# Kernel optimization log

Measured on AMD Instinct MI355X. Metric: run time of the kernel, lower is better.

## Reference

```python
import jax, jax.numpy as jnp
import numpy as np


def conv(x, w, b=None, stride=1, pad=0):
    out = jax.lax.conv_general_dilated(x, w, (stride, stride), [(pad, pad), (pad, pad)],
                                       dimension_numbers=('NCHW', 'OIHW', 'NCHW'))
    if b is not None:
        out = out + b[None, :, None, None]
    return out


def fsm(x, att_w, conv_w):
    # FeatureSelectionModule: global-avg-pool -> 1x1 conv -> sigmoid gate, residual, 1x1 proj
    gap = jnp.mean(x, axis=(2, 3), keepdims=True)
    atten = jax.nn.sigmoid(conv(gap, att_w))
    return conv(x + x * atten, conv_w)


def mdcn(x, offset, mask, weight, bias, pad=1, G=8):
    # Modulated deformable conv v2: stride 1, dilation 1, conv groups 1, G deformable groups.
    N, C, H, W = x.shape
    Co, Ci, kh, kw = weight.shape
    K = kh * kw
    Cg = C // G
    off = offset.reshape(N, G, 2, K, H, W)          # per-group (y, x) offsets per kernel tap
    msk = mask.reshape(N, G, 1, K, H, W)
    ky, kx = jnp.meshgrid(jnp.arange(kh), jnp.arange(kw), indexing='ij')
    py = (jnp.arange(H, dtype=x.dtype)[None, None, None, :, None] - pad) + ky.reshape(1, 1, K, 1, 1) + off[:, :, 0]
    px = (jnp.arange(W, dtype=x.dtype)[None, None, None, None, :] - pad) + kx.reshape(1, 1, K, 1, 1) + off[:, :, 1]
    y0 = jnp.floor(py)
    x0 = jnp.floor(px)
    wy1 = py - y0
    wy0 = 1.0 - wy1
    wx1 = px - x0
    wx0 = 1.0 - wx1
    xg = x.reshape(N, G, Cg, H * W)

    def gather(iy, ix):
        valid = (iy >= 0) & (iy <= H - 1) & (ix >= 0) & (ix <= W - 1)
        idx = (jnp.clip(iy, 0, H - 1) * W + jnp.clip(ix, 0, W - 1)).astype(jnp.int32)
        v = jnp.take_along_axis(xg, idx.reshape(N, G, 1, K * H * W), axis=3)
        return v.reshape(N, G, Cg, K, H, W) * valid[:, :, None].astype(x.dtype)

    val = ((wy0 * wx0)[:, :, None] * gather(y0, x0)
         + (wy0 * wx1)[:, :, None] * gather(y0, x0 + 1)
         + (wy1 * wx0)[:, :, None] * gather(y0 + 1, x0)
         + (wy1 * wx1)[:, :, None] * gather(y0 + 1, x0 + 1))
    val = val * msk                                   # [N,G,Cg,K,H,W]
    out = jnp.einsum('ngckhw,ogck->nohw', val, weight.reshape(Co, G, Cg, K))
    return out + bias[None, :, None, None]


def align(feat_l, feat_s, att_w, fsm_w, off_w, om_w, om_b, dcn_w, dcn_b):
    # FeatureAlign_V2
    N, Cs, H, W = feat_s.shape[0], feat_s.shape[1], feat_l.shape[2], feat_l.shape[3]
    feat_up = jax.image.resize(feat_s, (N, Cs, H, W), 'bilinear')  # align_corners=False
    feat_arm = fsm(feat_l, att_w, fsm_w)
    off_feat = conv(jnp.concatenate([feat_arm, feat_up * 2.0], axis=1), off_w)
    om = conv(off_feat, om_w, om_b, pad=1)            # conv_offset_mask: 3*G*K channels
    o1, o2, mk = jnp.split(om, 3, axis=1)
    offset = jnp.concatenate([o1, o2], axis=1)
    mask = jax.nn.sigmoid(mk)
    feat_align = jax.nn.relu(mdcn(feat_up, offset, mask, dcn_w, dcn_b))
    return feat_align + feat_arm


def setup_inputs() -> dict:
    key = jax.random.key(0)
    ks = iter(jax.random.split(key, 64))

    def w(shape):
        fan_in = shape[1] * shape[2] * shape[3]
        return jax.random.normal(next(ks), shape, jnp.float32) / np.float32(np.sqrt(fan_in))

    def b(n):
        return jnp.zeros((n,), jnp.float32)

    d = {}
    d['c2'] = jax.random.normal(next(ks), (1, 256, 128, 128), jnp.float32)
    d['c3'] = jax.random.normal(next(ks), (1, 512, 64, 64), jnp.float32)
    d['c4'] = jax.random.normal(next(ks), (1, 1024, 32, 32), jnp.float32)
    d['c5'] = jax.random.normal(next(ks), (1, 2048, 16, 16), jnp.float32)
    OC = 256
    OM = 8 * 3 * 9  # deformable_groups * (2 offsets + 1 mask) * k*k = 216
    for tag, in_nc in (('16', 1024), ('8', 512), ('4', 256)):
        d['att_w' + tag] = w((in_nc, in_nc, 1, 1))
        d['fsm_w' + tag] = w((OC, in_nc, 1, 1))
        d['off_w' + tag] = w((OC, 2 * OC, 1, 1))
        d['om_w' + tag] = w((OM, OC, 3, 3))
        d['om_b' + tag] = b(OM)
        d['dcn_w' + tag] = w((OC, OC, 3, 3))
        d['dcn_b' + tag] = b(OC)
        d['out_w' + tag] = w((OC, OC, 3, 3))
        d['out_b' + tag] = b(OC)
    d['lat_w'] = w((OC, 2048, 1, 1))
    d['lat_b'] = b(OC)
    return d


def reference(c2, c3, c4, c5,
              att_w16, fsm_w16, off_w16, om_w16, om_b16, dcn_w16, dcn_b16, out_w16, out_b16,
              att_w8, fsm_w8, off_w8, om_w8, om_b8, dcn_w8, dcn_b8, out_w8, out_b8,
              att_w4, fsm_w4, off_w4, om_w4, om_b4, dcn_w4, dcn_b4, out_w4, out_b4,
              lat_w, lat_b):
    # top-down pass, coarsest first (matches FAN.forward with reversed inputs)
    p5 = conv(c5, lat_w, lat_b)
    f16 = align(c4, p5, att_w16, fsm_w16, off_w16, om_w16, om_b16, dcn_w16, dcn_b16)
    p4 = conv(f16, out_w16, out_b16, pad=1)
    f8 = align(c3, f16, att_w8, fsm_w8, off_w8, om_w8, om_b8, dcn_w8, dcn_b8)
    p3 = conv(f8, out_w8, out_b8, pad=1)
    f4 = align(c2, f8, att_w4, fsm_w4, off_w4, om_w4, om_b4, dcn_w4, dcn_b4)
    p2 = conv(f4, out_w4, out_b4, pad=1)
    return (p2, p3, p4, p5)
```

## Files before the change

kernel.cpp:

```cpp
#include <hip/hip_runtime.h>
#include <hip/hip_bf16.h>

typedef __hip_bfloat16 bf16;
typedef __attribute__((ext_vector_type(8))) short bf16x8;
typedef __attribute__((ext_vector_type(4))) float floatx4;

__device__ __forceinline__ float b2f(bf16 v) { return __bfloat162float(v); }
__device__ __forceinline__ bf16 f2b(float v) { return __float2bfloat16(v); }
__device__ __forceinline__ float us2f(unsigned short u) {
  union { unsigned int i; float f; } v; v.i = ((unsigned int)u) << 16; return v.f;
}
__device__ __forceinline__ unsigned short f2us(float f) {
  bf16 h = f2b(f); return *(unsigned short*)&h;
}

__global__ __launch_bounds__(256) void gap_kernel(const float* __restrict__ x,
                                                  float* __restrict__ gap,
                                                  int HW, float inv) {
  int c = blockIdx.x;
  const float* p = x + (size_t)c * HW;
  float s = 0.f;
  for (int i = threadIdx.x; i < HW; i += 256) s += p[i];
  __shared__ float red[256];
  red[threadIdx.x] = s;
  __syncthreads();
  for (int w = 128; w > 0; w >>= 1) {
    if (threadIdx.x < w) red[threadIdx.x] += red[threadIdx.x + w];
    __syncthreads();
  }
  if (threadIdx.x == 0) gap[c] = red[0] * inv;
}

__global__ __launch_bounds__(256) void atten_kernel(const float* __restrict__ w,
                                                    const float* __restrict__ gap,
                                                    float* __restrict__ scale, int Ci) {
  int wave = threadIdx.x >> 6, lane = threadIdx.x & 63;
  int o = blockIdx.x * 4 + wave;
  const float4* wr = (const float4*)(w + (size_t)o * Ci);
  const float4* g4 = (const float4*)gap;
  int n4 = Ci >> 2;
  float s = 0.f;
  for (int i = lane; i < n4; i += 64) {
    float4 a = wr[i], b = g4[i];
    s += a.x * b.x + a.y * b.y + a.z * b.z + a.w * b.w;
  }
#pragma unroll
  for (int off = 32; off > 0; off >>= 1) s += __shfl_down(s, off);
  if (lane == 0) scale[o] = 1.f + 1.f / (1.f + expf(-s));
}

__global__ __launch_bounds__(256) void upsample2x_nhwc_kernel(
    const bf16* __restrict__ src, bf16* __restrict__ dst, int Hs, int Ws) {
  int p = blockIdx.x;
  int c = threadIdx.x;
  int W = Ws * 2;
  int y = p / W, x = p - y * W;
  float fy = y * 0.5f - 0.25f;
  float fx = x * 0.5f - 0.25f;
  int y0 = (int)floorf(fy), x0 = (int)floorf(fx);
  float wy1 = fy - (float)y0, wx1 = fx - (float)x0;
  int y0c = min(max(y0, 0), Hs - 1);
  int y1c = min(max(y0 + 1, 0), Hs - 1);
  int x0c = min(max(x0, 0), Ws - 1);
  int x1c = min(max(x0 + 1, 0), Ws - 1);
  float v00 = b2f(src[(size_t)(y0c * Ws + x0c) * 256 + c]);
  float v01 = b2f(src[(size_t)(y0c * Ws + x1c) * 256 + c]);
  float v10 = b2f(src[(size_t)(y1c * Ws + x0c) * 256 + c]);
  float v11 = b2f(src[(size_t)(y1c * Ws + x1c) * 256 + c]);
  float v = (1.f - wy1) * ((1.f - wx1) * v00 + wx1 * v01)
          + wy1 * ((1.f - wx1) * v10 + wx1 * v11);
  dst[(size_t)p * 256 + c] = f2b(v);
}

__global__ __launch_bounds__(256) void packw1_kernel(const float* __restrict__ w,
                                                     bf16* __restrict__ BP, int K) {
  int idx = blockIdx.x * 256 + threadIdx.x;
  int j = idx & 7;
  int o = (idx >> 3) & 255;
  int kc8 = idx >> 11;
  int k = kc8 * 8 + j;
  BP[idx] = f2b(w[(size_t)o * K + k]);
}

__global__ __launch_bounds__(256) void packwd_kernel(const float* __restrict__ w,
                                                     bf16* __restrict__ BP) {
  int idx = blockIdx.x * 256 + threadIdx.x;
  int j = idx & 7;
  int o = (idx >> 3) & 255;
  int k8 = idx >> 11;
  int k = k8 * 8 + j;
  int tap = k >> 8;
  int ci = k & 255;
  BP[idx] = f2b(w[((size_t)o * 256 + ci) * 9 + tap]);
}

__global__ __launch_bounds__(256) void packw3_kernel(const float* __restrict__ w,
                                                     bf16* __restrict__ BP,
                                                     int Ci, int Co) {
  int idx = blockIdx.x * 256 + threadIdx.x;
  int total = Ci * 9 * 256;
  if (idx >= total) return;
  int j = idx & 7;
  int t1 = idx >> 3;
  int o = t1 & 255;
  int t2 = t1 >> 8;
  int q = t2 & 3;
  int t3 = t2 >> 2;
  int tap = t3 % 9;
  int c = t3 / 9;
  int ci = c * 32 + q * 8 + j;
  float v = (o < Co) ? w[((size_t)o * Ci + ci) * 9 + tap] : 0.f;
  BP[idx] = f2b(v);
}

template <bool NCHW1, typename TA1>
__global__ __launch_bounds__(256) void conv1x1_mfma_kernel(
    const TA1* __restrict__ A1, const float* __restrict__ scaleA,
    const bf16* __restrict__ A2, float scaleB,
    int Ci1, int Ci2, int HW,
    const bf16* __restrict__ BP, const float* __restrict__ bias,
    float* __restrict__ out1, bf16* __restrict__ out2, int ns2) {
  __shared__ __align__(16) bf16 sA[1024];
  int p0 = blockIdx.x * 32;
  int tid = threadIdx.x;
  int pix = tid & 31, sub = tid >> 5;
  int pix2 = tid >> 3, sub8 = tid & 7;
  int lane = tid & 63, wave = tid >> 6;
  int pg = wave & 1, cg = wave >> 1;
  int q = lane >> 4, n = lane & 15;

  floatx4 acc[4];
#pragma unroll
  for (int nt = 0; nt < 4; ++nt) acc[nt] = (floatx4)0.f;

  int nch = (Ci1 + Ci2) >> 5;
  for (int kc = 0; kc < nch; ++kc) {
    int ci0 = kc << 5;
    if (NCHW1 && ci0 < Ci1) {
#pragma unroll
      for (int it = 0; it < 4; ++it) {
        int cil = it * 8 + sub;
        float x = (float)A1[(size_t)(ci0 + cil) * HW + p0 + pix];
        if (scaleA) x *= scaleA[ci0 + cil];
        sA[((cil >> 3) * 32 + pix) * 8 + (cil & 7)] = f2b(x);
      }
    } else {
      const bf16* src; int cb; bool scl;
      if (!NCHW1 && ci0 < Ci1) {
        src = (const bf16*)(const void*)A1; cb = ci0; scl = false;
      } else {
        src = A2; cb = ci0 - Ci1; scl = true;
      }
      ushort4 raw = *(const ushort4*)&src[(size_t)(p0 + pix2) * 256 + cb + sub8 * 4];
      if (scl) {
        raw.x = f2us(us2f(raw.x) * scaleB);
        raw.y = f2us(us2f(raw.y) * scaleB);
        raw.z = f2us(us2f(raw.z) * scaleB);
        raw.w = f2us(us2f(raw.w) * scaleB);
      }
      *(ushort4*)&sA[((sub8 >> 1) * 32 + pix2) * 8 + (sub8 & 1) * 4] = raw;
    }
    __syncthreads();
    bf16x8 a = *(const bf16x8*)&sA[(q * 32 + pg * 16 + n) * 8];
    const bf16* bp = BP + ((size_t)(kc * 4 + q) * 256 + blockIdx.y * 128 + cg * 64) * 8;
#pragma unroll
    for (int nt = 0; nt < 4; ++nt) {
      bf16x8 b = *(const bf16x8*)&bp[(nt * 16 + n) * 8];
      acc[nt] = __builtin_amdgcn_mfma_f32_16x16x32_bf16(a, b, acc[nt], 0, 0, 0);
    }
    __syncthreads();
  }

  int pbase = p0 + pg * 16 + q * 4;
#pragma unroll
  for (int nt = 0; nt < 4; ++nt) {
    int o = blockIdx.y * 128 + cg * 64 + nt * 16 + n;
    float bv = bias ? bias[o] : 0.f;
#pragma unroll
    for (int r = 0; r < 4; ++r) {
      float v = acc[nt][r] + bv;
      if (out1) out1[(size_t)o * HW + pbase + r] = v;
      if (out2) out2[(size_t)(pbase + r) * ns2 + o] = f2b(v);
    }
  }
}

__global__ __launch_bounds__(256) void conv1x1_part_kernel(
    const float* __restrict__ A1, int HW,
    const bf16* __restrict__ BP, float* __restrict__ PART) {
  __shared__ __align__(16) bf16 sA[1024];
  int p0 = blockIdx.x * 32;
  int tid = threadIdx.x;
  int pix = tid & 31, sub = tid >> 5;
  int lane = tid & 63, wave = tid >> 6;
  int pg = wave & 1, cg = wave >> 1;
  int q = lane >> 4, n = lane & 15;

  floatx4 acc[4];
#pragma unroll
  for (int nt = 0; nt < 4; ++nt) acc[nt] = (floatx4)0.f;

  int kc0 = blockIdx.z * 8;
  for (int kcl = 0; kcl < 8; ++kcl) {
    int kc = kc0 + kcl;
    int ci0 = kc << 5;
#pragma unroll
    for (int it = 0; it < 4; ++it) {
      int cil = it * 8 + sub;
      sA[((cil >> 3) * 32 + pix) * 8 + (cil & 7)] =
          f2b(A1[(size_t)(ci0 + cil) * HW + p0 + pix]);
    }
    __syncthreads();
    bf16x8 a = *(const bf16x8*)&sA[(q * 32 + pg * 16 + n) * 8];
    const bf16* bp = BP + ((size_t)(kc * 4 + q) * 256 + blockIdx.y * 128 + cg * 64) * 8;
#pragma unroll
    for (int nt = 0; nt < 4; ++nt) {
      bf16x8 b = *(const bf16x8*)&bp[(nt * 16 + n) * 8];
      acc[nt] = __builtin_amdgcn_mfma_f32_16x16x32_bf16(a, b, acc[nt], 0, 0, 0);
    }
    __syncthreads();
  }

  int pbase = p0 + pg * 16 + q * 4;
#pragma unroll
  for (int nt = 0; nt < 4; ++nt) {
    int o = blockIdx.y * 128 + cg * 64 + nt * 16 + n;
#pragma unroll
    for (int r = 0; r < 4; ++r)
      PART[((size_t)blockIdx.z * 256 + o) * HW + pbase + r] = acc[nt][r];
  }
}

__global__ __launch_bounds__(256) void reduce_p5_kernel(
    const float* __restrict__ PART, const float* __restrict__ bias,
    float* __restrict__ out1, bf16* __restrict__ out2, int HW, int KS) {
  int o = blockIdx.x;
  int p = threadIdx.x;
  float s = bias[o];
  for (int z = 0; z < KS; ++z) s += PART[((size_t)z * 256 + o) * HW + p];
  out1[(size_t)o * HW + p] = s;
  out2[(size_t)p * 256 + o] = f2b(s);
}

__global__ __launch_bounds__(256) void conv3x3_mfma_kernel(
    const bf16* __restrict__ in, const bf16* __restrict__ BP,
    const float* __restrict__ bias,
    int H, int W, int Co,
    float* __restrict__ out1, bf16* __restrict__ out2, int ns2) {
  __shared__ __align__(16) bf16 sA[9216];
  int HW = H * W;
  int segs = W >> 5;
  int y = blockIdx.x / segs;
  int x0 = (blockIdx.x - y * segs) << 5;
  int tid = threadIdx.x;
  int pix2 = tid >> 3, sub8 = tid & 7;
  int lane = tid & 63, wave = tid >> 6;
  int pg = wave & 1, cg = wave >> 1;
  int q = lane >> 4, n = lane & 15;

  floatx4 acc[4];
#pragma unroll
  for (int nt = 0; nt < 4; ++nt) acc[nt] = (floatx4)0.f;

  int xx = x0 + pix2;
  for (int kc = 0; kc < 8; ++kc) {
    int ci0 = kc << 5;
#pragma unroll
    for (int tap = 0; tap < 9; ++tap) {
      int dy = tap / 3 - 1, dx = tap % 3 - 1;
      int yy = y + dy, xg = xx + dx;
      ushort4 v = {0, 0, 0, 0};
      if ((unsigned)yy < (unsigned)H && (unsigned)xg < (unsigned)W)
        v = *(const ushort4*)&in[(size_t)(yy * W + xg) * 256 + ci0 + sub8 * 4];
      *(ushort4*)&sA[((tap * 4 + (sub8 >> 1)) * 32 + pix2) * 8 + (sub8 & 1) * 4] = v;
    }
    __syncthreads();
    const bf16* bpc = BP + (size_t)kc * 73728;
#pragma unroll
    for (int tap = 0; tap < 9; ++tap) {
      bf16x8 a = *(const bf16x8*)&sA[((tap * 4 + q) * 32 + pg * 16 + n) * 8];
      const bf16* bp =
          bpc + ((size_t)(tap * 4 + q) * 256 + blockIdx.y * 128 + cg * 64) * 8;
#pragma unroll
      for (int nt = 0; nt < 4; ++nt) {
        bf16x8 b = *(const bf16x8*)&bp[(nt * 16 + n) * 8];
        acc[nt] = __builtin_amdgcn_mfma_f32_16x16x32_bf16(a, b, acc[nt], 0, 0, 0);
      }
    }
    __syncthreads();
  }

  int pbase = y * W + x0 + pg * 16 + q * 4;
#pragma unroll
  for (int nt = 0; nt < 4; ++nt) {
    int o = blockIdx.y * 128 + cg * 64 + nt * 16 + n;
    if (o < Co) {
      float bv = bias ? bias[o] : 0.f;
#pragma unroll
      for (int r = 0; r < 4; ++r) {
        float v = acc[nt][r] + bv;
        if (out1) out1[(size_t)o * HW + pbase + r] = v;
        if (out2) out2[(size_t)(pbase + r) * ns2 + o] = f2b(v);
      }
    }
  }
}

__global__ __launch_bounds__(512, 4) void mdcn_mfma_kernel(
    const bf16* __restrict__ UPn, const bf16* __restrict__ OM,
    const bf16* __restrict__ BP, const float* __restrict__ dcn_b,
    const bf16* __restrict__ ARM, bf16* __restrict__ F,
    int H, int W, int wshift) {
  __shared__ __align__(16) bf16 sval[2][32 * 272];
  __shared__ float4 mw[2304];
  __shared__ int mi[2304];
  int pb = blockIdx.x * 32;
  int tid = threadIdx.x;

  for (int t2 = tid; t2 < 2304; t2 += 512) {
    int px_ = t2 & 31, g = (t2 >> 5) & 7, tap = t2 >> 8;
    int ky = tap / 3, kx = tap - ky * 3;
    int p = pb + px_;
    int y = p >> wshift, x = p & (W - 1);
    const bf16* omp = OM + (size_t)p * 216;
    float dy = b2f(omp[g * 18 + tap]);
    float dx = b2f(omp[g * 18 + 9 + tap]);
    float mm = 1.f / (1.f + expf(-b2f(omp[144 + g * 9 + tap])));
    float fpy = (float)(y - 1 + ky) + dy;
    float fpx = (float)(x - 1 + kx) + dx;
    fpy = fminf(fmaxf(fpy, -1.0e4f), 1.0e4f);
    fpx = fminf(fmaxf(fpx, -1.0e4f), 1.0e4f);
    float fy0 = floorf(fpy), fx0 = floorf(fpx);
    float wy1 = fpy - fy0, wx1 = fpx - fx0;
    float wy0 = 1.f - wy1, wx0 = 1.f - wx1;
    int iy0 = (int)fy0, ix0 = (int)fx0;
    bool vy0 = (unsigned)iy0 < (unsigned)H;
    bool vy1 = (unsigned)(iy0 + 1) < (unsigned)H;
    bool vx0 = (unsigned)ix0 < (unsigned)W;
    bool vx1 = (unsigned)(ix0 + 1) < (unsigned)W;
    float w00 = (vy0 && vx0) ? mm * wy0 * wx0 : 0.f;
    float w01 = (vy0 && vx1) ? mm * wy0 * wx1 : 0.f;
    float w10 = (vy1 && vx0) ? mm * wy1 * wx0 : 0.f;
    float w11 = (vy1 && vx1) ? mm * wy1 * wx1 : 0.f;
    int iy0c = min(max(iy0, 0), H - 1);
    int iy1c = min(max(iy0 + 1, 0), H - 1);
    int ix0c = min(max(ix0, 0), W - 1);
    int ix1c = min(max(ix0 + 1, 0), W - 1);
    mw[t2] = make_float4(w00, w01, w10, w11);
    mi[t2] = (iy0c * W + ix0c) | ((ix1c - ix0c) << 20) | ((iy1c - iy0c) << 21);
  }
  __syncthreads();

  int px = tid >> 4, l2 = tid & 15;
  int lane = tid & 63, wave = tid >> 6;
  int q = lane >> 4, n = lane & 15;
  int rowb = l2 >> 2;
  int woff = px * 8 + (l2 & 3) * 2;

  floatx4 acc[2][2];
#pragma unroll
  for (int m = 0; m < 2; ++m)
#pragma unroll
    for (int nt = 0; nt < 2; ++nt) acc[m][nt] = (floatx4)0.f;

  auto gather = [&](int t) {
    bf16* sv = &sval[t & 1][0];
    int base = t * 256 + px;
#pragma unroll
    for (int g = 0; g < 8; ++g) {
      float4 wv = mw[base + g * 32];
      int mv = mi[base + g * 32];
      int idx = mv & 0x3FFFF;
      int dxs = (mv >> 20) & 1;
      int dyW = ((mv >> 21) & 1) * W;
      const bf16* up = UPn + (size_t)idx * 256 + g * 32 + l2 * 2;
      ushort2 u00 = *(const ushort2*)(up);
      ushort2 u01 = *(const ushort2*)(up + dxs * 256);
      ushort2 u10 = *(const ushort2*)(up + dyW * 256);
      ushort2 u11 = *(const ushort2*)(up + (dyW + dxs) * 256);
      float s0 = wv.x * us2f(u00.x) + wv.y * us2f(u01.x)
               + wv.z * us2f(u10.x) + wv.w * us2f(u11.x);
      float s1 = wv.x * us2f(u00.y) + wv.y * us2f(u01.y)
               + wv.z * us2f(u10.y) + wv.w * us2f(u11.y);
      ushort2 o2;
      o2.x = f2us(s0);
      o2.y = f2us(s1);
      *(ushort2*)&sv[(g * 4 + rowb) * 272 + woff] = o2;
    }
  };

  gather(0);
  for (int t = 0; t < 9; ++t) {
    __syncthreads();
    if (t < 8) gather(t + 1);
    const bf16* sv = &sval[t & 1][0];
    const bf16* bpt = BP + ((size_t)(t * 32) * 256 + wave * 32) * 8;
#pragma unroll
    for (int kc = 0; kc < 8; ++kc) {
      int R = kc * 4 + q;
      bf16x8 a0 = *(const bf16x8*)&sv[R * 272 + n * 8];
      bf16x8 a1 = *(const bf16x8*)&sv[R * 272 + (16 + n) * 8];
      const bf16* bp = bpt + (size_t)R * 2048;
      bf16x8 b0 = *(const bf16x8*)&bp[n * 8];
      bf16x8 b1 = *(const bf16x8*)&bp[(16 + n) * 8];
      acc[0][0] = __builtin_amdgcn_mfma_f32_16x16x32_bf16(a0, b0, acc[0][0], 0, 0, 0);
      acc[0][1] = __builtin_amdgcn_mfma_f32_16x16x32_bf16(a0, b1, acc[0][1], 0, 0, 0);
      acc[1][0] = __builtin_amdgcn_mfma_f32_16x16x32_bf16(a1, b0, acc[1][0], 0, 0, 0);
      acc[1][1] = __builtin_amdgcn_mfma_f32_16x16x32_bf16(a1, b1, acc[1][1], 0, 0, 0);
    }
  }

#pragma unroll
  for (int m = 0; m < 2; ++m) {
#pragma unroll
    for (int nt = 0; nt < 2; ++nt) {
      int o = wave * 32 + nt * 16 + n;
      float bv = dcn_b[o];
#pragma unroll
      for (int r = 0; r < 4; ++r) {
        int p = pb + m * 16 + q * 4 + r;
        float v = fmaxf(acc[m][nt][r] + bv, 0.f) + b2f(ARM[(size_t)p * 256 + o]);
        F[(size_t)p * 256 + o] = f2b(v);
      }
    }
  }
}

extern "C" void kernel_launch(void* const* d_in, const int* in_sizes, int n_in,
                              void* d_out, int out_size, void* d_ws, size_t ws_size,
                              hipStream_t stream) {
  const float* c2 = (const float*)d_in[0];
  const float* c3 = (const float*)d_in[1];
  const float* c4 = (const float*)d_in[2];
  const float* c5 = (const float*)d_in[3];
  const float* lat_w = (const float*)d_in[31];
  const float* lat_b = (const float*)d_in[32];
  float* out = (float*)d_out;
  (void)ws_size; (void)in_sizes; (void)n_in; (void)out_size;

  const size_t p2_off = 0;
  const size_t p3_off = 4194304;
  const size_t p4_off = p3_off + 1048576;
  const size_t p5_off = p4_off + 262144;

  char* ws = (char*)d_ws;
  bf16* UPn = (bf16*)(ws);
  bf16* ARM = (bf16*)(ws + 8388608);
  bf16* FB  = (bf16*)(ws + 16777216);
  bf16* P5N = (bf16*)(ws + 25165824);
  bf16* BPB = (bf16*)(ws + 25296896);
  float* GAP = (float*)(ws + 26476544);
  float* SC  = (float*)(ws + 26484736);
  bf16* OM = (bf16*)(out + p2_off);
  float* PART = (float*)ws;

  packw1_kernel<<<2048, 256, 0, stream>>>(lat_w, BPB, 2048);
  conv1x1_part_kernel<<<dim3(8, 2, 8), 256, 0, stream>>>(c5, 256, BPB, PART);
  reduce_p5_kernel<<<256, 256, 0, stream>>>(PART, lat_b, out + p5_off, P5N, 256, 8);

  struct Lv {
    const float* featl; int Ci; int H; int W; int wshift;
    float* pdst; int wbase;
  };
  Lv levels[3] = {
      {c4, 1024, 32, 32, 5, out + p4_off, 4},
      {c3, 512, 64, 64, 6, out + p3_off, 13},
      {c2, 256, 128, 128, 7, out + p2_off, 22},
  };

  for (int li = 0; li < 3; ++li) {
    const Lv& L = levels[li];
    const float* att_w = (const float*)d_in[L.wbase + 0];
    const float* fsm_w = (const float*)d_in[L.wbase + 1];
    const float* off_w = (const float*)d_in[L.wbase + 2];
    const float* om_w  = (const float*)d_in[L.wbase + 3];
    const float* om_b  = (const float*)d_in[L.wbase + 4];
    const float* dcn_w = (const float*)d_in[L.wbase + 5];
    const float* dcn_b = (const float*)d_in[L.wbase + 6];
    const float* out_w = (const float*)d_in[L.wbase + 7];
    const float* out_b = (const float*)d_in[L.wbase + 8];
    int HW = L.H * L.W;

    upsample2x_nhwc_kernel<<<HW, 256, 0, stream>>>(
        (li == 0) ? P5N : FB, UPn, L.H / 2, L.W / 2);
    gap_kernel<<<L.Ci, 256, 0, stream>>>(L.featl, GAP, HW, 1.f / (float)HW);
    atten_kernel<<<L.Ci / 4, 256, 0, stream>>>(att_w, GAP, SC, L.Ci);
    packw1_kernel<<<L.Ci, 256, 0, stream>>>(fsm_w, BPB, L.Ci);
    conv1x1_mfma_kernel<true, float><<<dim3(HW / 32, 2), 256, 0, stream>>>(
        L.featl, SC, nullptr, 0.f, L.Ci, 0, HW, BPB, nullptr,
        nullptr, ARM, 256);
    packw1_kernel<<<512, 256, 0, stream>>>(off_w, BPB, 512);
    conv1x1_mfma_kernel<false, bf16><<<dim3(HW / 32, 2), 256, 0, stream>>>(
        ARM, nullptr, UPn, 2.f, 256, 256, HW, BPB, nullptr,
        nullptr, FB, 256);
    packw3_kernel<<<2304, 256, 0, stream>>>(om_w, BPB, 256, 216);
    conv3x3_mfma_kernel<<<dim3(HW / 32, 2), 256, 0, stream>>>(
        FB, BPB, om_b, L.H, L.W, 216, nullptr, OM, 216);
    packwd_kernel<<<2304, 256, 0, stream>>>(dcn_w, BPB);
    mdcn_mfma_kernel<<<HW / 32, 512, 0, stream>>>(
        UPn, OM, BPB, dcn_b, ARM, FB, L.H, L.W, L.wshift);
    packw3_kernel<<<2304, 256, 0, stream>>>(out_w, BPB, 256, 256);
    conv3x3_mfma_kernel<<<dim3(HW / 32, 2), 256, 0, stream>>>(
        FB, BPB, out_b, L.H, L.W, 256, L.pdst, nullptr, 256);
  }
}
```

Before: 777.5 us.

## Restructure 3x3 conv with halo tile reuse, double-buffered LDS and wider pixel tiles

The 3x3 conv kernel now stages a 3-row halo tile once per channel chunk and reads each tap from it with shifted offsets, instead of loading a separate copy of the input for every tap. Loads for the next channel chunk are prefetched into registers and written into a second LDS buffer, so global loads overlap with MFMA work and there is one barrier per chunk instead of two. On the largest level each block covers 64 pixels, reusing each weight fragment across two MFMA tiles. This costs more registers and LDS per block and gives fewer blocks on the largest level.

```diff
diff --git a/kernel.cpp b/kernel.cpp
--- a/kernel.cpp
+++ b/kernel.cpp
@@ -242,65 +242,109 @@
   out2[(size_t)p * 256 + o] = f2b(s);
 }
 
-__global__ __launch_bounds__(256) void conv3x3_mfma_kernel(
+template <int S>
+__global__ __launch_bounds__(256) void conv3x3v2_kernel(
     const bf16* __restrict__ in, const bf16* __restrict__ BP,
     const float* __restrict__ bias,
     int H, int W, int Co,
     float* __restrict__ out1, bf16* __restrict__ out2, int ns2) {
-  __shared__ __align__(16) bf16 sA[9216];
+  constexpr int P = 32 * S + 2;
+  constexpr int TASKS = 3 * P * 8;
+  constexpr int ITS = (TASKS + 255) / 256;
+  __shared__ __align__(16) bf16 sA[2][4 * 3 * P * 8];
   int HW = H * W;
-  int segs = W >> 5;
+  int segs = W / (32 * S);
   int y = blockIdx.x / segs;
-  int x0 = (blockIdx.x - y * segs) << 5;
+  int x0 = (blockIdx.x - y * segs) * (32 * S);
   int tid = threadIdx.x;
-  int pix2 = tid >> 3, sub8 = tid & 7;
   int lane = tid & 63, wave = tid >> 6;
   int pg = wave & 1, cg = wave >> 1;
   int q = lane >> 4, n = lane & 15;
 
-  floatx4 acc[4];
-#pragma unroll
-  for (int nt = 0; nt < 4; ++nt) acc[nt] = (floatx4)0.f;
-
-  int xx = x0 + pix2;
+  int dstIdx[ITS], srcOff[ITS];
+  bool act[ITS], val[ITS];
+#pragma unroll
+  for (int it = 0; it < ITS; ++it) {
+    int tt = it * 256 + tid;
+    act[it] = (tt < TASKS);
+    int sub8 = tt & 7;
+    int rp = tt >> 3;
+    int row = rp / P;
+    int pxl = rp - row * P;
+    int yy = y + row - 1;
+    int xg = x0 + pxl - 1;
+    bool v = act[it] && ((unsigned)yy < (unsigned)H) && ((unsigned)xg < (unsigned)W);
+    val[it] = v;
+    srcOff[it] = v ? ((yy * W + xg) * 256 + sub8 * 4) : 0;
+    dstIdx[it] = (((sub8 >> 1) * 3 + row) * P + pxl) * 8 + (sub8 & 1) * 4;
+  }
+
+  ushort4 pv[ITS];
+  auto load_regs = [&](int kc) {
+    int cb = kc << 5;
+#pragma unroll
+    for (int it = 0; it < ITS; ++it) {
+      ushort4 z = {0, 0, 0, 0};
+      pv[it] = val[it] ? *(const ushort4*)&in[(size_t)srcOff[it] + cb] : z;
+    }
+  };
+  auto store_lds = [&](int buf) {
+#pragma unroll
+    for (int it = 0; it < ITS; ++it)
+      if (act[it]) *(ushort4*)&sA[buf][dstIdx[it]] = pv[it];
+  };
+
+  floatx4 acc[S][4];
+#pragma unroll
+  for (int s = 0; s < S; ++s)
+#pragma unroll
+    for (int nt = 0; nt < 4; ++nt) acc[s][nt] = (floatx4)0.f;
+
+  load_regs(0);
+  store_lds(0);
+  __syncthreads();
+  load_regs(1);
+
   for (int kc = 0; kc < 8; ++kc) {
-    int ci0 = kc << 5;
+    const bf16* sv = &sA[kc & 1][0];
+    const bf16* bpc = BP + (size_t)kc * 73728;
 #pragma unroll
     for (int tap = 0; tap < 9; ++tap) {
-      int dy = tap / 3 - 1, dx = tap % 3 - 1;
-      int yy = y + dy, xg = xx + dx;
-      ushort4 v = {0, 0, 0, 0};
-      if ((unsigned)yy < (unsigned)H && (unsigned)xg < (unsigned)W)
-        v = *(const ushort4*)&in[(size_t)(yy * W + xg) * 256 + ci0 + sub8 * 4];
-      *(ushort4*)&sA[((tap * 4 + (sub8 >> 1)) * 32 + pix2) * 8 + (sub8 & 1) * 4] = v;
-    }
-    __syncthreads();
-    const bf16* bpc = BP + (size_t)kc * 73728;
-#pragma unroll
-    for (int tap = 0; tap < 9; ++tap) {
-      bf16x8 a = *(const bf16x8*)&sA[((tap * 4 + q) * 32 + pg * 16 + n) * 8];
-      const bf16* bp =
-          bpc + ((size_t)(tap * 4 + q) * 256 + blockIdx.y * 128 + cg * 64) * 8;
+      int ty = tap / 3, tx = tap % 3;
+      bf16x8 a[S];
+#pragma unroll
+      for (int s = 0; s < S; ++s)
+        a[s] = *(const bf16x8*)&sv[((q * 3 + ty) * P + tx + s * 32 + pg * 16 + n) * 8];
+      const bf16* bp = bpc + ((size_t)(tap * 4 + q) * 256 + blockIdx.y * 128 + cg * 64) * 8;
 #pragma unroll
       for (int nt = 0; nt < 4; ++nt) {
         bf16x8 b = *(const bf16x8*)&bp[(nt * 16 + n) * 8];
-        acc[nt] = __builtin_amdgcn_mfma_f32_16x16x32_bf16(a, b, acc[nt], 0, 0, 0);
+#pragma unroll
+        for (int s = 0; s < S; ++s)
+          acc[s][nt] = __builtin_amdgcn_mfma_f32_16x16x32_bf16(a[s], b, acc[s][nt], 0, 0, 0);
       }
     }
-    __syncthreads();
-  }
-
-  int pbase = y * W + x0 + pg * 16 + q * 4;
-#pragma unroll
-  for (int nt = 0; nt < 4; ++nt) {
-    int o = blockIdx.y * 128 + cg * 64 + nt * 16 + n;
-    if (o < Co) {
-      float bv = bias ? bias[o] : 0.f;
-#pragma unroll
-      for (int r = 0; r < 4; ++r) {
-        float v = acc[nt][r] + bv;
-        if (out1) out1[(size_t)o * HW + pbase + r] = v;
-        if (out2) out2[(size_t)(pbase + r) * ns2 + o] = f2b(v);
+    if (kc < 7) {
+      store_lds((kc + 1) & 1);
+      __syncthreads();
+      if (kc < 6) load_regs(kc + 2);
+    }
+  }
+
+#pragma unroll
+  for (int s = 0; s < S; ++s) {
+    int pbase = y * W + x0 + s * 32 + pg * 16 + q * 4;
+#pragma unroll
+    for (int nt = 0; nt < 4; ++nt) {
+      int o = blockIdx.y * 128 + cg * 64 + nt * 16 + n;
+      if (o < Co) {
+        float bv = bias ? bias[o] : 0.f;
+#pragma unroll
+        for (int r = 0; r < 4; ++r) {
+          float v = acc[s][nt][r] + bv;
+          if (out1) out1[(size_t)o * HW + pbase + r] = v;
+          if (out2) out2[(size_t)(pbase + r) * ns2 + o] = f2b(v);
+        }
       }
     }
   }
@@ -494,13 +538,21 @@
         ARM, nullptr, UPn, 2.f, 256, 256, HW, BPB, nullptr,
         nullptr, FB, 256);
     packw3_kernel<<<2304, 256, 0, stream>>>(om_w, BPB, 256, 216);
-    conv3x3_mfma_kernel<<<dim3(HW / 32, 2), 256, 0, stream>>>(
-        FB, BPB, om_b, L.H, L.W, 216, nullptr, OM, 216);
+    if (li == 2)
+      conv3x3v2_kernel<2><<<dim3(HW / 64, 2), 256, 0, stream>>>(
+          FB, BPB, om_b, L.H, L.W, 216, nullptr, OM, 216);
+    else
+      conv3x3v2_kernel<1><<<dim3(HW / 32, 2), 256, 0, stream>>>(
+          FB, BPB, om_b, L.H, L.W, 216, nullptr, OM, 216);
     packwd_kernel<<<2304, 256, 0, stream>>>(dcn_w, BPB);
     mdcn_mfma_kernel<<<HW / 32, 512, 0, stream>>>(
         UPn, OM, BPB, dcn_b, ARM, FB, L.H, L.W, L.wshift);
     packw3_kernel<<<2304, 256, 0, stream>>>(out_w, BPB, 256, 256);
-    conv3x3_mfma_kernel<<<dim3(HW / 32, 2), 256, 0, stream>>>(
-        FB, BPB, out_b, L.H, L.W, 256, L.pdst, nullptr, 256);
-  }
-}
+    if (li == 2)
+      conv3x3v2_kernel<2><<<dim3(HW / 64, 2), 256, 0, stream>>>(
+          FB, BPB, out_b, L.H, L.W, 256, L.pdst, nullptr, 256);
+    else
+      conv3x3v2_kernel<1><<<dim3(HW / 32, 2), 256, 0, stream>>>(
+          FB, BPB, out_b, L.H, L.W, 256, L.pdst, nullptr, 256);
+  }
+}
```

New measurement: 733.3 us. -5.7%, faster.
